# Kernel tuning notes

Hardware: AMD Instinct MI355X
Metric: run time of the kernel (lower is better)

## Reference

```python
import jax, jax.numpy as jnp
import numpy as np

N_NODES = 50000
N_EDGES = 800000
F_IN, F_HID, F_OUT = 128, 256, 128


def setup_inputs() -> dict:
    key = jax.random.key(0)
    ks = jax.random.split(key, 16)
    inp = {
        "x": jax.random.normal(ks[0], (N_NODES, F_IN), dtype=jnp.float32),
        "edge0": jax.random.randint(ks[1], (2, N_EDGES), 0, N_NODES, dtype=jnp.int64),
        "edge1": jax.random.randint(ks[2], (2, N_EDGES), 0, N_NODES, dtype=jnp.int64),
        "edge2": jax.random.randint(ks[3], (2, N_EDGES), 0, N_NODES, dtype=jnp.int64),
    }
    dims = [(F_IN, F_HID), (F_HID, F_HID), (F_HID, F_OUT)]
    for i, (di, do) in enumerate(dims):
        inp[f"Wl{i}"] = 0.02 * jax.random.normal(ks[4 + 3 * i], (di, do), dtype=jnp.float32)
        inp[f"bl{i}"] = jnp.zeros((do,), dtype=jnp.float32)
        inp[f"Wr{i}"] = 0.02 * jax.random.normal(ks[5 + 3 * i], (di, do), dtype=jnp.float32)
    return inp


def _sage_layer(x, src, dst, Wl, bl, Wr):
    # gather source features, mean-aggregate into destinations
    msg = x[src]                                            # [E, F]
    agg = jax.ops.segment_sum(msg, dst, num_segments=N_NODES)
    cnt = jax.ops.segment_sum(jnp.ones((src.shape[0], 1), x.dtype), dst,
                              num_segments=N_NODES)
    mean = agg / jnp.maximum(cnt, 1.0)
    # PyG SAGEConv: lin_l(aggr) + lin_r(x_self); lin_r has no bias
    return mean @ Wl + bl + x @ Wr


def reference(x, edge0, edge1, edge2, Wl0, bl0, Wr0, Wl1, bl1, Wr1, Wl2, bl2, Wr2):
    # vstack-swap + flow='target_to_source' == aggregate edge[0] -> edge[1]
    edges = [edge0, edge1, edge2]
    params = [(Wl0, bl0, Wr0), (Wl1, bl1, Wr1), (Wl2, bl2, Wr2)]
    h = x
    for e, (Wl, bl, Wr) in zip(edges, params):
        h = _sage_layer(h, e[0], e[1], Wl, bl, Wr)
        h = jax.nn.relu(h)
        # dropout skipped (eval mode)
    return h
```

## Files before the change

### kernel.cpp

```cpp
#include <hip/hip_runtime.h>
#include <hip/hip_bf16.h>
#include <stdint.h>

#define N_NODES 50000
#define N_EDGES 800000
#define NBG 196
#define MG 3125
#define MG64 782
#define EG4 782

typedef __attribute__((ext_vector_type(8))) short short8;
typedef __attribute__((ext_vector_type(4))) float floatx4;

__device__ __forceinline__ float bfbits2f(unsigned int u16) {
    union { unsigned int i; float f; } c; c.i = u16 << 16; return c.f;
}
__device__ __forceinline__ unsigned short f2bfbits(float f) {
    union { float f; unsigned int i; } c; c.f = f;
    unsigned int r = c.i + 0x7fffu + ((c.i >> 16) & 1u);
    return (unsigned short)(r >> 16);
}
__device__ __forceinline__ void acc8(float* a, uint4 v) {
    a[0] += bfbits2f(v.x & 0xffffu); a[1] += bfbits2f(v.x >> 16);
    a[2] += bfbits2f(v.y & 0xffffu); a[3] += bfbits2f(v.y >> 16);
    a[4] += bfbits2f(v.z & 0xffffu); a[5] += bfbits2f(v.z >> 16);
    a[6] += bfbits2f(v.w & 0xffffu); a[7] += bfbits2f(v.w >> 16);
}

#define GATHER_RUN(IDX)                                                        \
    {                                                                          \
        int j = 0;                                                             \
        for (; j + 15 < deg; j += 16) {                                        \
            uint4 vv[16];                                                      \
            _Pragma("unroll")                                                  \
            for (int u = 0; u < 16; ++u)                                       \
                vv[u] = *(const uint4*)(col + (size_t)IDX(j + u) * K);         \
            _Pragma("unroll")                                                  \
            for (int u = 0; u < 16; ++u) acc8((u & 1) ? g : a, vv[u]);         \
        }                                                                      \
        for (; j + 7 < deg; j += 8) {                                          \
            uint4 vv[8];                                                       \
            _Pragma("unroll")                                                  \
            for (int u = 0; u < 8; ++u)                                        \
                vv[u] = *(const uint4*)(col + (size_t)IDX(j + u) * K);         \
            _Pragma("unroll")                                                  \
            for (int u = 0; u < 8; ++u) acc8((u & 1) ? g : a, vv[u]);          \
        }                                                                      \
        for (; j + 1 < deg; j += 2) {                                          \
            uint4 v0 = *(const uint4*)(col + (size_t)IDX(j) * K);              \
            uint4 v1 = *(const uint4*)(col + (size_t)IDX(j + 1) * K);          \
            acc8(a, v0); acc8(g, v1);                                          \
        }                                                                      \
        if (j < deg) {                                                         \
            uint4 v0 = *(const uint4*)(col + (size_t)IDX(j) * K);              \
            acc8(a, v0);                                                       \
        }                                                                      \
    }

__device__ __forceinline__ void count4_body(
    int blk, int tid, const int* __restrict__ e, int* __restrict__ rp,
    int* __restrict__ rank, int f1, int useRank)
{
#pragma unroll
    for (int u = 0; u < 4; ++u) {
        int i = blk * 1024 + u * 256 + tid;
        if (i < N_EDGES) {
            int dst = f1 ? e[2 * (N_EDGES + i)] : e[N_EDGES + i];
            if (useRank) rank[i] = atomicAdd(&rp[dst], 1);
            else         atomicAdd(&rp[dst], 1);
        }
    }
}

__device__ __forceinline__ void fill4_body(
    int blk, int tid, const int* __restrict__ e, int* __restrict__ rp,
    const int* __restrict__ part, int* __restrict__ csr,
    const int* __restrict__ rank, int f1, int useRank)
{
#pragma unroll
    for (int u = 0; u < 4; ++u) {
        int i = blk * 1024 + u * 256 + tid;
        if (i < N_EDGES) {
            int src = f1 ? e[2 * i] : e[i];
            int dst = f1 ? e[2 * (N_EDGES + i)] : e[N_EDGES + i];
            int pos;
            if (useRank) pos = part[dst >> 8] + rp[dst] + rank[i];
            else         pos = part[dst >> 8] + atomicAdd(&rp[dst], 1);
            csr[pos] = src;
        }
    }
}

__device__ __forceinline__ int srp_load(
    int m0, int tid, const int* __restrict__ rp, const int* __restrict__ part,
    int useRank)
{
    int r0 = m0 + tid - (useRank ? 0 : 1);
    if (r0 < 0) return 0;
    if (r0 >= N_NODES) return N_EDGES;
    return rp[r0] + part[r0 >> 8];
}

__global__ __launch_bounds__(256) void mega1(
    const void* __restrict__ Wl0, const void* __restrict__ Wr0,
    const void* __restrict__ Wl1, const void* __restrict__ Wr1,
    const void* __restrict__ Wl2, const void* __restrict__ Wr2,
    const void* __restrict__ b0, const void* __restrict__ b1, const void* __restrict__ b2,
    unsigned short* __restrict__ wt,
    const void* __restrict__ x, unsigned short* __restrict__ xb,
    const int* __restrict__ e0,
    int* __restrict__ rp0, int* __restrict__ rank, int useRank,
    int* __restrict__ flagsOut)
{
    __shared__ int s_cnt[2];
    const int t = threadIdx.x;
    if (t < 2) s_cnt[t] = 0;
    __syncthreads();
    {
        unsigned short v = ((const unsigned short*)x)[2 * t];
        int ex = (v >> 7) & 0xff;
        unsigned long long m0 = __ballot(v == 0 || (ex >= 96 && ex <= 150));
        unsigned long long m1 = __ballot(e0[2 * t + 1] != 0);
        if ((t & 63) == 0) {
            atomicAdd(&s_cnt[0], (int)__popcll(m0));
            atomicAdd(&s_cnt[1], (int)__popcll(m1));
        }
    }
    __syncthreads();
    const int f0 = (s_cnt[0] < 200) ? 1 : 0;
    const int f1 = (s_cnt[1] < 128) ? 1 : 0;
    const int bid = blockIdx.x;

    if (bid == 8059) {
        if (t == 0) { flagsOut[0] = f0; flagsOut[1] = f1; }
        return;
    }
    if (bid >= 7277) {
        count4_body(bid - 7277, t, e0, rp0, rank, f1, useRank);
        return;
    }
    if (bid >= 1027) {
        int i = (bid - 1027) * 256 + t;
        if (f0) {
            float4 v = ((const float4*)x)[i];
            uint2 o;
            o.x = (unsigned int)f2bfbits(v.x) | ((unsigned int)f2bfbits(v.y) << 16);
            o.y = (unsigned int)f2bfbits(v.z) | ((unsigned int)f2bfbits(v.w) << 16);
            ((uint2*)xb)[i] = o;
        } else {
            ((uint2*)xb)[i] = ((const uint2*)x)[i];
        }
        return;
    }
    if (bid >= 1024) {
        const void* bs = bid == 1024 ? b0 : (bid == 1025 ? b1 : b2);
        unsigned short* bd = wt + 262144 + (bid - 1024) * 256;
        int n = (bid == 1026) ? 128 : 256;
        if (t < n) bd[t] = f0 ? f2bfbits(((const float*)bs)[t]) : ((const unsigned short*)bs)[t];
        return;
    }
    const void* W; unsigned short* WT; int Nd, SK, KO, off;
    if (bid < 128)      { W = Wl0; WT = wt;          Nd = 256; off = bid;       SK = 256; KO = 0;   }
    else if (bid < 256) { W = Wr0; WT = wt;          Nd = 256; off = bid - 128; SK = 256; KO = 128; }
    else if (bid < 512) { W = Wl1; WT = wt + 65536;  Nd = 256; off = bid - 256; SK = 512; KO = 0;   }
    else if (bid < 768) { W = Wr1; WT = wt + 65536;  Nd = 256; off = bid - 512; SK = 512; KO = 256; }
    else if (bid < 896) { W = Wl2; WT = wt + 196608; Nd = 128; off = bid - 768; SK = 256; KO = 0;   }
    else                { W = Wr2; WT = wt + 229376; Nd = 128; off = bid - 896; SK = 256; KO = 0;   }
    int idx = off * 256 + t;
    int k = idx / Nd, n = idx - k * Nd;
    unsigned short v = f0 ? f2bfbits(((const float*)W)[idx]) : ((const unsigned short*)W)[idx];
    WT[n * SK + KO + k] = v;
}

__global__ __launch_bounds__(256) void scan_g(
    int* __restrict__ rp, int* __restrict__ part, int* __restrict__ ticket)
{
    __shared__ int sa[256], sb[256];
    __shared__ int lastBlk;
    const int b = blockIdx.x, t = threadIdx.x, idx = b * 256 + t;
    int v = (idx < N_NODES) ? rp[idx] : 0;
    sa[t] = v;
    __syncthreads();
    bool par = true;
#pragma unroll
    for (int off = 1; off < 256; off <<= 1) {
        if (par) { int x2 = sa[t] + (t >= off ? sa[t - off] : 0); sb[t] = x2; }
        else     { int x2 = sb[t] + (t >= off ? sb[t - off] : 0); sa[t] = x2; }
        par = !par;
        __syncthreads();
    }
    if (idx < N_NODES) rp[idx] = sa[t] - v;
    if (t == 255) part[b] = sa[255];
    __threadfence();
    if (t == 0) lastBlk = (atomicAdd(ticket, 1) == (int)gridDim.x - 1) ? 1 : 0;
    __syncthreads();
    if (!lastBlk) return;

    int pv = (t < NBG) ? atomicAdd(&part[t], 0) : 0;
    sa[t] = pv;
    __syncthreads();
    par = true;
#pragma unroll
    for (int off = 1; off < 256; off <<= 1) {
        if (par) { int x2 = sa[t] + (t >= off ? sa[t - off] : 0); sb[t] = x2; }
        else     { int x2 = sb[t] + (t >= off ? sb[t - off] : 0); sa[t] = x2; }
        par = !par;
        __syncthreads();
    }
    if (t < NBG) part[t] = sa[t] - pv;
}

__global__ __launch_bounds__(256) void fill_k(
    const int* __restrict__ e, int* __restrict__ rp, const int* __restrict__ part,
    int* __restrict__ csr, const int* __restrict__ rank, int useRank,
    const int* __restrict__ flags)
{
    fill4_body(blockIdx.x, threadIdx.x, e, rp, part, csr, rank, flags[1], useRank);
}

template<int K, int OSTR>
__global__ __launch_bounds__(256) void gath(
    const unsigned short* __restrict__ hin,
    const int* __restrict__ rp, const int* __restrict__ part,
    const int* __restrict__ csr_src,
    unsigned short* __restrict__ mout,
    const int* __restrict__ eN, int* __restrict__ rpN,
    int* __restrict__ rankN, int useRank,
    const int* __restrict__ flags)
{
    constexpr int CH = K / 8;
    constexpr int CAP = 1024;
    __shared__ int sidx[CAP];
    __shared__ int srp[17];
    const int tid = threadIdx.x;
    if (blockIdx.x < EG4) {
        count4_body(blockIdx.x, tid, eN, rpN, rankN, flags[1], useRank);
        return;
    }
    const int m0 = (blockIdx.x - EG4) * 16;
    if (tid < 17) srp[tid] = srp_load(m0, tid, rp, part, useRank);
    __syncthreads();
    const int base = srp[0];
    const int total = srp[16] - base;
    const bool staged = total <= CAP;
    if (staged) {
        for (int i = tid; i < total; i += 256) sidx[i] = csr_src[base + i];
    }
    __syncthreads();

    for (int it = tid; it < 16 * CH; it += 256) {
        const int rr = it / CH;
        const int cc = it & (CH - 1);
        const int beg = srp[rr];
        const int deg = srp[rr + 1] - beg;
        const int begl = beg - base;
        float a[8], g[8];
#pragma unroll
        for (int v = 0; v < 8; ++v) { a[v] = 0.f; g[v] = 0.f; }
        const unsigned short* col = hin + cc * 8;
        if (staged) {
            auto IDX = [&](int j) { return sidx[begl + j]; };
            GATHER_RUN(IDX)
        } else {
            auto IDX = [&](int j) { return csr_src[beg + j]; };
            GATHER_RUN(IDX)
        }
        const float inv = 1.0f / fmaxf((float)deg, 1.0f);
        short8 t8;
#pragma unroll
        for (int v = 0; v < 8; ++v) t8[v] = (short)f2bfbits((a[v] + g[v]) * inv);
        *(short8*)(mout + (size_t)(m0 + rr) * OSTR + cc * 8) = t8;
    }
}

template<int K>
__global__ __launch_bounds__(256) void gemmcat(
    const unsigned short* __restrict__ mean, int mstr,
    const unsigned short* __restrict__ self, int sstr,
    const unsigned short* __restrict__ WcatT,
    const unsigned short* __restrict__ bb,
    unsigned short* __restrict__ hout,
    const int* __restrict__ ef, int* __restrict__ rpf, const int* __restrict__ partf,
    int* __restrict__ csr, const int* __restrict__ rank, int useRank,
    const int* __restrict__ flags)
{
    constexpr int KE = 2 * K;
    constexpr int KH = 128;
    constexpr int NKH = KE / KH;
    constexpr int LDA = KH + 8;
    __shared__ unsigned short A[64][LDA];
    const int tid = threadIdx.x;
    if (blockIdx.x < EG4) {
        fill4_body(blockIdx.x, tid, ef, rpf, partf, csr, rank, flags[1], useRank);
        return;
    }
    const int m0 = (blockIdx.x - EG4) * 64;
    const int lane = tid & 63, wave = tid >> 6;
    const int r = lane & 15, quad = lane >> 4;

    floatx4 acc[4][4] = {};

#pragma unroll
    for (int kh = 0; kh < NKH; ++kh) {
        if (kh) __syncthreads();
        for (int i = tid; i < 64 * (KH / 8); i += 256) {
            const int row = i / (KH / 8);
            const int c8 = i - row * (KH / 8);
            int grow = m0 + row; if (grow >= N_NODES) grow = N_NODES - 1;
            const int gc = kh * KH + c8 * 8;
            const unsigned short* src = (gc < K)
                ? (mean + (size_t)grow * mstr + gc)
                : (self + (size_t)grow * sstr + (gc - K));
            *(uint4*)&A[row][c8 * 8] = *(const uint4*)src;
        }
        __syncthreads();
#pragma unroll
        for (int nti = 0; nti < 4; ++nti) {
            const int n0 = (wave + nti * 4) * 16;
            short8 bf[KH / 32];
            const unsigned short* bp = WcatT + (size_t)(n0 + r) * KE + kh * KH + quad * 8;
#pragma unroll
            for (int k0 = 0; k0 < KH / 32; ++k0) bf[k0] = *(const short8*)(bp + k0 * 32);
#pragma unroll
            for (int mt = 0; mt < 4; ++mt) {
#pragma unroll
                for (int k0 = 0; k0 < KH / 32; ++k0)
                    acc[nti][mt] = __builtin_amdgcn_mfma_f32_16x16x32_bf16(
                        *(const short8*)&A[mt * 16 + r][k0 * 32 + quad * 8],
                        bf[k0], acc[nti][mt], 0, 0, 0);
            }
        }
    }

#pragma unroll
    for (int nti = 0; nti < 4; ++nti) {
        const int ccol = (wave + nti * 4) * 16 + r;
        const float bv = bfbits2f(bb[ccol]);
#pragma unroll
        for (int mt = 0; mt < 4; ++mt) {
#pragma unroll
            for (int i = 0; i < 4; ++i) {
                const int row = m0 + mt * 16 + quad * 4 + i;
                float v = acc[nti][mt][i] + bv;
                v = v > 0.f ? v : 0.f;
                if (row < N_NODES) hout[(size_t)row * 256 + ccol] = f2bfbits(v);
            }
        }
    }
}

__global__ __launch_bounds__(256) void gemmL2(
    const unsigned short* __restrict__ A,
    const unsigned short* __restrict__ WT,
    unsigned short* __restrict__ out0,
    unsigned short* __restrict__ out1)
{
    __shared__ unsigned short As[64][264];
    const int tid = threadIdx.x;
    const int m0 = blockIdx.x * 64;
    for (int i = tid; i < 64 * 32; i += 256) {
        int rr = i >> 5, cc = i & 31;
        int row = m0 + rr; if (row >= N_NODES) row = N_NODES - 1;
        *(uint4*)&As[rr][cc * 8] = *(const uint4*)(A + (size_t)row * 256 + cc * 8);
    }
    __syncthreads();
    const int lane = tid & 63, wave = tid >> 6;
    const int r = lane & 15, quad = lane >> 4;

    for (int nt = wave; nt < 16; nt += 4) {
        const int n0 = nt * 16;
        short8 bf[8];
        const unsigned short* bp = WT + (size_t)(n0 + r) * 256 + quad * 8;
#pragma unroll
        for (int k0 = 0; k0 < 8; ++k0) bf[k0] = *(const short8*)(bp + k0 * 32);
        const int ccol = n0 + r;
#pragma unroll
        for (int mt = 0; mt < 4; ++mt) {
            floatx4 acc = {0.f, 0.f, 0.f, 0.f};
#pragma unroll
            for (int k0 = 0; k0 < 8; ++k0)
                acc = __builtin_amdgcn_mfma_f32_16x16x32_bf16(
                    *(const short8*)&As[mt * 16 + r][k0 * 32 + quad * 8], bf[k0], acc, 0, 0, 0);
#pragma unroll
            for (int i = 0; i < 4; ++i) {
                const int row = m0 + mt * 16 + quad * 4 + i;
                if (row < N_NODES) {
                    unsigned short v = f2bfbits(acc[i]);
                    if (ccol < 128) out0[(size_t)row * 128 + ccol] = v;
                    else            out1[(size_t)row * 128 + ccol - 128] = v;
                }
            }
        }
    }
}

__global__ __launch_bounds__(256) void agg2(
    const unsigned short* __restrict__ hl2,
    const unsigned short* __restrict__ hr2,
    const int* __restrict__ rp, const int* __restrict__ part,
    const int* __restrict__ csr_src,
    const unsigned short* __restrict__ bb,
    void* __restrict__ out, int useRank,
    const int* __restrict__ flags)
{
    constexpr int K = 128, CAP = 3072;
    __shared__ int sidx[CAP];
    __shared__ int srp[17];
    const int tid = threadIdx.x;
    const int m0 = blockIdx.x * 16;
    if (tid < 17) srp[tid] = srp_load(m0, tid, rp, part, useRank);
    __syncthreads();
    const int base = srp[0];
    const int total = srp[16] - base;
    const bool staged = total <= CAP;
    if (staged) {
        for (int i = tid; i < total; i += 256) sidx[i] = csr_src[base + i];
    }
    __syncthreads();

    const int rr = tid >> 4;
    const int cc = tid & 15;
    const int beg = srp[rr];
    const int deg = srp[rr + 1] - beg;
    const int begl = beg - base;
    float a[8], g[8];
#pragma unroll
    for (int v = 0; v < 8; ++v) { a[v] = 0.f; g[v] = 0.f; }
    const unsigned short* col = hl2 + cc * 8;
    if (staged) {
        auto IDX = [&](int j) { return sidx[begl + j]; };
        GATHER_RUN(IDX)
    } else {
        auto IDX = [&](int j) { return csr_src[beg + j]; };
        GATHER_RUN(IDX)
    }

    const float inv = 1.0f / fmaxf((float)deg, 1.0f);
    const size_t ro = (size_t)(m0 + rr) * K + cc * 8;
    uint4 hv = *(const uint4*)(hr2 + ro);
    uint4 bv = *(const uint4*)(bb + cc * 8);
    float h8[8], b8[8];
    h8[0] = bfbits2f(hv.x & 0xffffu); h8[1] = bfbits2f(hv.x >> 16);
    h8[2] = bfbits2f(hv.y & 0xffffu); h8[3] = bfbits2f(hv.y >> 16);
    h8[4] = bfbits2f(hv.z & 0xffffu); h8[5] = bfbits2f(hv.z >> 16);
    h8[6] = bfbits2f(hv.w & 0xffffu); h8[7] = bfbits2f(hv.w >> 16);
    b8[0] = bfbits2f(bv.x & 0xffffu); b8[1] = bfbits2f(bv.x >> 16);
    b8[2] = bfbits2f(bv.y & 0xffffu); b8[3] = bfbits2f(bv.y >> 16);
    b8[4] = bfbits2f(bv.z & 0xffffu); b8[5] = bfbits2f(bv.z >> 16);
    b8[6] = bfbits2f(bv.w & 0xffffu); b8[7] = bfbits2f(bv.w >> 16);
    float o8[8];
#pragma unroll
    for (int v = 0; v < 8; ++v) {
        float m = (a[v] + g[v]) * inv + b8[v] + h8[v];
        o8[v] = m > 0.f ? m : 0.f;
    }
    if (flags[0]) {
        float* op = (float*)out + ro;
        float4 o0 = { o8[0], o8[1], o8[2], o8[3] };
        float4 o1 = { o8[4], o8[5], o8[6], o8[7] };
        *(float4*)op = o0;
        *(float4*)(op + 4) = o1;
    } else {
        short8 t8;
#pragma unroll
        for (int v = 0; v < 8; ++v) t8[v] = (short)f2bfbits(o8[v]);
        *(short8*)((unsigned short*)out + ro) = t8;
    }
}

extern "C" void kernel_launch(void* const* d_in, const int* in_sizes, int n_in,
                              void* d_out, int out_size, void* d_ws, size_t ws_size,
                              hipStream_t stream) {
    const void* x  = d_in[0];
    const int* e[3] = { (const int*)d_in[1], (const int*)d_in[2], (const int*)d_in[3] };

    char* ws = (char*)d_ws;
    int* flags = (int*)ws;
    unsigned short* wt = (unsigned short*)(ws + 1024);
    unsigned short* bb0 = wt + 262144;
    unsigned short* bb1 = wt + 262400;
    unsigned short* bb2 = wt + 262656;
    int* rp3    = (int*)(ws + 526592);
    int* ticket = (int*)(ws + 1126592);
    int* part3  = (int*)(ws + 1126604);
    int* csr    = (int*)(ws + 1128960);
    unsigned short* hA = (unsigned short*)(ws + 4328960);
    unsigned short* hB = (unsigned short*)(ws + 29928960);
    int* rank  = (int*)(ws + 55528960);
    unsigned short* xb  = hB;
    unsigned short* hl2 = hA;
    unsigned short* hr2 = hA + (size_t)N_NODES * 128;

    const int useRank = (ws_size >= (size_t)58728960) ? 1 : 0;

    int* rp0 = rp3, * rp1 = rp3 + N_NODES, * rp2 = rp3 + 2 * N_NODES;
    int* pt0 = part3, * pt1 = part3 + NBG, * pt2 = part3 + 2 * NBG;

    hipMemsetAsync(rp3, 0, 600012, stream);
    mega1<<<8060, 256, 0, stream>>>(d_in[4], d_in[6], d_in[7], d_in[9],
                                    d_in[10], d_in[12], d_in[5], d_in[8], d_in[11],
                                    wt, x, xb, e[0], rp0, rank, useRank, flags);
    scan_g<<<NBG, 256, 0, stream>>>(rp0, pt0, ticket + 0);
    fill_k<<<EG4, 256, 0, stream>>>(e[0], rp0, pt0, csr, rank, useRank, flags);
    gath<128, 256><<<EG4 + MG, 256, 0, stream>>>(xb, rp0, pt0, csr, hA,
                                                 e[1], rp1, rank, useRank, flags);
    scan_g<<<NBG, 256, 0, stream>>>(rp1, pt1, ticket + 1);
    gemmcat<128><<<EG4 + MG64, 256, 0, stream>>>(hA, 256, xb, 128,
                                                 wt, bb0, hA,
                                                 e[1], rp1, pt1, csr, rank, useRank, flags);
    gath<256, 256><<<EG4 + MG, 256, 0, stream>>>(hA, rp1, pt1, csr, hB,
                                                 e[2], rp2, rank, useRank, flags);
    scan_g<<<NBG, 256, 0, stream>>>(rp2, pt2, ticket + 2);
    gemmcat<256><<<EG4 + MG64, 256, 0, stream>>>(hB, 256, hA, 256,
                                                 wt + 65536, bb1, hB,
                                                 e[2], rp2, pt2, csr, rank, useRank, flags);
    gemmL2<<<MG64, 256, 0, stream>>>(hB, wt + 196608, hl2, hr2);
    agg2<<<MG, 256, 0, stream>>>(hl2, hr2, rp2, pt2, csr, bb2, d_out, useRank, flags);
}
```

Baseline: 514.6 us.

## Fuse mean-gather with concat GEMM per 32-row tile; re-home CSR fill kernels

Merges the gather/mean kernel and the concat GEMM into one kernel. Each block aggregates 32 destination rows into shared memory next to their self features, then runs MFMA directly from LDS. This removes the round trip of the mean matrix through global memory and one launch per layer. The CSR fill work for the next layer moves out of the GEMM: layer 1's fill becomes a separate launch and layer 2's fill piggybacks on the final GEMM kernel. The trade-offs are higher LDS use per block, which lowers occupancy during the latency-bound gather, fewer rows per GEMM tile, and the 16-wide gather unroll is dropped.

```diff
diff --git a/kernel.cpp b/kernel.cpp
--- a/kernel.cpp
+++ b/kernel.cpp
@@ -6,6 +6,7 @@
 #define N_EDGES 800000
 #define NBG 196
 #define MG 3125
+#define MG32 1563
 #define MG64 782
 #define EG4 782
 
@@ -30,14 +31,6 @@
 #define GATHER_RUN(IDX)                                                        \
     {                                                                          \
         int j = 0;                                                             \
-        for (; j + 15 < deg; j += 16) {                                        \
-            uint4 vv[16];                                                      \
-            _Pragma("unroll")                                                  \
-            for (int u = 0; u < 16; ++u)                                       \
-                vv[u] = *(const uint4*)(col + (size_t)IDX(j + u) * K);         \
-            _Pragma("unroll")                                                  \
-            for (int u = 0; u < 16; ++u) acc8((u & 1) ? g : a, vv[u]);         \
-        }                                                                      \
         for (; j + 7 < deg; j += 8) {                                          \
             uint4 vv[8];                                                       \
             _Pragma("unroll")                                                  \
@@ -218,37 +211,48 @@
     fill4_body(blockIdx.x, threadIdx.x, e, rp, part, csr, rank, flags[1], useRank);
 }
 
-template<int K, int OSTR>
-__global__ __launch_bounds__(256) void gath(
+template<int K>
+__global__ __launch_bounds__(256) void fused_lay(
     const unsigned short* __restrict__ hin,
+    const unsigned short* __restrict__ selfp, int sstr,
     const int* __restrict__ rp, const int* __restrict__ part,
     const int* __restrict__ csr_src,
-    unsigned short* __restrict__ mout,
+    const unsigned short* __restrict__ WcatT,
+    const unsigned short* __restrict__ bb,
+    unsigned short* __restrict__ hout,
     const int* __restrict__ eN, int* __restrict__ rpN,
     int* __restrict__ rankN, int useRank,
     const int* __restrict__ flags)
 {
     constexpr int CH = K / 8;
+    constexpr int KE = 2 * K;
+    constexpr int LDA = KE + 8;
     constexpr int CAP = 1024;
+    __shared__ unsigned short A[32][LDA];
     __shared__ int sidx[CAP];
-    __shared__ int srp[17];
+    __shared__ int srp[33];
     const int tid = threadIdx.x;
     if (blockIdx.x < EG4) {
         count4_body(blockIdx.x, tid, eN, rpN, rankN, flags[1], useRank);
         return;
     }
-    const int m0 = (blockIdx.x - EG4) * 16;
-    if (tid < 17) srp[tid] = srp_load(m0, tid, rp, part, useRank);
+    const int m0 = (blockIdx.x - EG4) * 32;
+    if (tid < 33) srp[tid] = srp_load(m0, tid, rp, part, useRank);
     __syncthreads();
     const int base = srp[0];
-    const int total = srp[16] - base;
+    const int total = srp[32] - base;
     const bool staged = total <= CAP;
     if (staged) {
         for (int i = tid; i < total; i += 256) sidx[i] = csr_src[base + i];
     }
-    __syncthreads();
-
-    for (int it = tid; it < 16 * CH; it += 256) {
+    for (int i = tid; i < 32 * CH; i += 256) {
+        int rr = i / CH, cc = i - rr * CH;
+        int row = m0 + rr; if (row >= N_NODES) row = N_NODES - 1;
+        *(uint4*)&A[rr][K + cc * 8] = *(const uint4*)(selfp + (size_t)row * sstr + cc * 8);
+    }
+    __syncthreads();
+
+    for (int it = tid; it < 32 * CH; it += 256) {
         const int rr = it / CH;
         const int cc = it & (CH - 1);
         const int beg = srp[rr];
@@ -269,64 +273,28 @@
         short8 t8;
 #pragma unroll
         for (int v = 0; v < 8; ++v) t8[v] = (short)f2bfbits((a[v] + g[v]) * inv);
-        *(short8*)(mout + (size_t)(m0 + rr) * OSTR + cc * 8) = t8;
-    }
-}
-
-template<int K>
-__global__ __launch_bounds__(256) void gemmcat(
-    const unsigned short* __restrict__ mean, int mstr,
-    const unsigned short* __restrict__ self, int sstr,
-    const unsigned short* __restrict__ WcatT,
-    const unsigned short* __restrict__ bb,
-    unsigned short* __restrict__ hout,
-    const int* __restrict__ ef, int* __restrict__ rpf, const int* __restrict__ partf,
-    int* __restrict__ csr, const int* __restrict__ rank, int useRank,
-    const int* __restrict__ flags)
-{
-    constexpr int KE = 2 * K;
-    constexpr int KH = 128;
-    constexpr int NKH = KE / KH;
-    constexpr int LDA = KH + 8;
-    __shared__ unsigned short A[64][LDA];
-    const int tid = threadIdx.x;
-    if (blockIdx.x < EG4) {
-        fill4_body(blockIdx.x, tid, ef, rpf, partf, csr, rank, flags[1], useRank);
-        return;
-    }
-    const int m0 = (blockIdx.x - EG4) * 64;
+        *(short8*)&A[rr][cc * 8] = t8;
+    }
+    __syncthreads();
+
     const int lane = tid & 63, wave = tid >> 6;
     const int r = lane & 15, quad = lane >> 4;
-
-    floatx4 acc[4][4] = {};
-
-#pragma unroll
-    for (int kh = 0; kh < NKH; ++kh) {
-        if (kh) __syncthreads();
-        for (int i = tid; i < 64 * (KH / 8); i += 256) {
-            const int row = i / (KH / 8);
-            const int c8 = i - row * (KH / 8);
-            int grow = m0 + row; if (grow >= N_NODES) grow = N_NODES - 1;
-            const int gc = kh * KH + c8 * 8;
-            const unsigned short* src = (gc < K)
-                ? (mean + (size_t)grow * mstr + gc)
-                : (self + (size_t)grow * sstr + (gc - K));
-            *(uint4*)&A[row][c8 * 8] = *(const uint4*)src;
-        }
-        __syncthreads();
-#pragma unroll
-        for (int nti = 0; nti < 4; ++nti) {
-            const int n0 = (wave + nti * 4) * 16;
-            short8 bf[KH / 32];
-            const unsigned short* bp = WcatT + (size_t)(n0 + r) * KE + kh * KH + quad * 8;
-#pragma unroll
-            for (int k0 = 0; k0 < KH / 32; ++k0) bf[k0] = *(const short8*)(bp + k0 * 32);
-#pragma unroll
-            for (int mt = 0; mt < 4; ++mt) {
-#pragma unroll
-                for (int k0 = 0; k0 < KH / 32; ++k0)
+    floatx4 acc[4][2] = {};
+#pragma unroll
+    for (int nti = 0; nti < 4; ++nti) {
+        const int n0 = (wave + nti * 4) * 16;
+        const unsigned short* bp = WcatT + (size_t)(n0 + r) * KE + quad * 8;
+#pragma unroll
+        for (int kh = 0; kh < KE / 128; ++kh) {
+            short8 bf[4];
+#pragma unroll
+            for (int k0 = 0; k0 < 4; ++k0) bf[k0] = *(const short8*)(bp + kh * 128 + k0 * 32);
+#pragma unroll
+            for (int mt = 0; mt < 2; ++mt) {
+#pragma unroll
+                for (int k0 = 0; k0 < 4; ++k0)
                     acc[nti][mt] = __builtin_amdgcn_mfma_f32_16x16x32_bf16(
-                        *(const short8*)&A[mt * 16 + r][k0 * 32 + quad * 8],
+                        *(const short8*)&A[mt * 16 + r][kh * 128 + k0 * 32 + quad * 8],
                         bf[k0], acc[nti][mt], 0, 0, 0);
             }
         }
@@ -337,7 +305,7 @@
         const int ccol = (wave + nti * 4) * 16 + r;
         const float bv = bfbits2f(bb[ccol]);
 #pragma unroll
-        for (int mt = 0; mt < 4; ++mt) {
+        for (int mt = 0; mt < 2; ++mt) {
 #pragma unroll
             for (int i = 0; i < 4; ++i) {
                 const int row = m0 + mt * 16 + quad * 4 + i;
@@ -349,15 +317,22 @@
     }
 }
 
-__global__ __launch_bounds__(256) void gemmL2(
+__global__ __launch_bounds__(256) void gemmL2f(
     const unsigned short* __restrict__ A,
     const unsigned short* __restrict__ WT,
     unsigned short* __restrict__ out0,
-    unsigned short* __restrict__ out1)
+    unsigned short* __restrict__ out1,
+    const int* __restrict__ e2, int* __restrict__ rp2, const int* __restrict__ pt2,
+    int* __restrict__ csr, const int* __restrict__ rank, int useRank,
+    const int* __restrict__ flags)
 {
     __shared__ unsigned short As[64][264];
     const int tid = threadIdx.x;
-    const int m0 = blockIdx.x * 64;
+    if (blockIdx.x < EG4) {
+        fill4_body(blockIdx.x, tid, e2, rp2, pt2, csr, rank, flags[1], useRank);
+        return;
+    }
+    const int m0 = (blockIdx.x - EG4) * 64;
     for (int i = tid; i < 64 * 32; i += 256) {
         int rr = i >> 5, cc = i & 31;
         int row = m0 + rr; if (row >= N_NODES) row = N_NODES - 1;
@@ -502,18 +477,16 @@
                                     wt, x, xb, e[0], rp0, rank, useRank, flags);
     scan_g<<<NBG, 256, 0, stream>>>(rp0, pt0, ticket + 0);
     fill_k<<<EG4, 256, 0, stream>>>(e[0], rp0, pt0, csr, rank, useRank, flags);
-    gath<128, 256><<<EG4 + MG, 256, 0, stream>>>(xb, rp0, pt0, csr, hA,
-                                                 e[1], rp1, rank, useRank, flags);
+    fused_lay<128><<<EG4 + MG32, 256, 0, stream>>>(xb, xb, 128, rp0, pt0, csr,
+                                                   wt, bb0, hA,
+                                                   e[1], rp1, rank, useRank, flags);
     scan_g<<<NBG, 256, 0, stream>>>(rp1, pt1, ticket + 1);
-    gemmcat<128><<<EG4 + MG64, 256, 0, stream>>>(hA, 256, xb, 128,
-                                                 wt, bb0, hA,
-                                                 e[1], rp1, pt1, csr, rank, useRank, flags);
-    gath<256, 256><<<EG4 + MG, 256, 0, stream>>>(hA, rp1, pt1, csr, hB,
-                                                 e[2], rp2, rank, useRank, flags);
+    fill_k<<<EG4, 256, 0, stream>>>(e[1], rp1, pt1, csr, rank, useRank, flags);
+    fused_lay<256><<<EG4 + MG32, 256, 0, stream>>>(hA, hA, 256, rp1, pt1, csr,
+                                                   wt + 65536, bb1, hB,
+                                                   e[2], rp2, rank, useRank, flags);
     scan_g<<<NBG, 256, 0, stream>>>(rp2, pt2, ticket + 2);
-    gemmcat<256><<<EG4 + MG64, 256, 0, stream>>>(hB, 256, hA, 256,
-                                                 wt + 65536, bb1, hB,
-                                                 e[2], rp2, pt2, csr, rank, useRank, flags);
-    gemmL2<<<MG64, 256, 0, stream>>>(hB, wt + 196608, hl2, hr2);
+    gemmL2f<<<EG4 + MG64, 256, 0, stream>>>(hB, wt + 196608, hl2, hr2,
+                                            e[2], rp2, pt2, csr, rank, useRank, flags);
     agg2<<<MG, 256, 0, stream>>>(hl2, hr2, rp2, pt2, csr, bb2, d_out, useRank, flags);
 }
```

Result: slower. 534.6 us (+3.9%).
